# Performance work log

Measured on AMD Instinct MI355X. Metric: run time of the kernel, lower is better.

Reference implementation:

```python
import jax, jax.numpy as jnp
import numpy as np
import math

BS, S, D, H = 16, 512, 1024, 16
DK = D // H
HALF = H // 2
R, GAMMA, EPS = 1.0, 0.1, 1e-6


def _alibi(n_heads, maxpos):
    # n_heads=16 is a power of 2
    start = 2.0 ** (-2.0 ** (-(math.log2(n_heads) - 3)))
    slopes = np.array([start * start ** i for i in range(n_heads)], dtype=np.float32) * -1.0
    pos = np.arange(maxpos)
    rel = np.abs(pos[None, :] - pos[:, None]).astype(np.float32)
    return jnp.asarray((slopes[:, None, None] * rel)[None])  # (1,H,maxpos,maxpos)


def setup_inputs() -> dict:
    key = jax.random.key(0)
    ks = jax.random.split(key, 6)
    sc = 1.0 / math.sqrt(D)
    x = jax.random.normal(ks[0], (BS, S, D), dtype=jnp.float32)
    Wq = jax.random.normal(ks[1], (D, D), dtype=jnp.float32) * sc
    Wk = jax.random.normal(ks[2], (D, D), dtype=jnp.float32) * sc
    Wv = jax.random.normal(ks[3], (D, D), dtype=jnp.float32) * sc
    Wo = jax.random.normal(ks[4], (D, D), dtype=jnp.float32) * sc
    bq = jnp.zeros((D,), jnp.float32)
    bk = jnp.zeros((D,), jnp.float32)
    bv = jnp.zeros((D,), jnp.float32)
    bo = jnp.zeros((D,), jnp.float32)
    alibi = _alibi(H, S)  # pre-sliced to seq_len (original slices [:,:,:S,:S])
    # src_mask for mask=0: np.triu(ones,k=0)==0 -> strictly lower triangular
    mask = jnp.tril(jnp.ones((S, S), dtype=bool), k=-1)[None, None]
    return {"x": x, "Wq": Wq, "bq": bq, "Wk": Wk, "bk": bk, "Wv": Wv,
            "bv": bv, "Wo": Wo, "bo": bo, "alibi": alibi, "mask": mask}


def _map_psi(x, r):
    x_y = jax.nn.sigmoid(x[..., -1])           # (b,h,s)
    return x[..., :-1] * x_y[..., None] * r, x_y * r


def _penumbral(q, k, r=R, gamma=GAMMA, eps=EPS):
    q_x, q_y = _map_psi(q, r)
    k_x, k_y = _map_psi(k, r)
    q_y = q_y[..., :, None]                    # (b,h,s,1)
    k_y = k_y[..., None, :]                    # (b,h,1,s)
    x_q_y = jnp.sqrt(r ** 2 - q_y ** 2 + eps)
    x_k_y = jnp.sqrt(r ** 2 - k_y ** 2 + eps)
    # euclidean cdist over last dim (d_k-1)
    qn = jnp.sum(q_x ** 2, axis=-1)[..., :, None]
    kn = jnp.sum(k_x ** 2, axis=-1)[..., None, :]
    d2 = qn + kn - 2.0 * jnp.einsum('bhqd,bhkd->bhqk', q_x, k_x)
    pd = jnp.sqrt(jnp.maximum(d2, 0.0) + 1e-12)
    lca = jnp.maximum(jnp.maximum(q_y ** 2, k_y ** 2),
                      r ** 2 - ((x_q_y + x_k_y - pd) / 2.0) ** 2)
    lca_out = ((pd ** 2 + k_y ** 2 - q_y ** 2) / (2.0 * pd + eps)) ** 2 + q_y ** 2
    exists = (pd <= x_q_y) | ((pd - x_q_y) ** 2 + k_y ** 2 <= r ** 2)
    return -gamma * jnp.where(exists, lca, lca_out)


def _masked_softmax_zeropad(scores, mask):
    scores = jnp.where(mask, scores, -1e32)
    p = jax.nn.softmax(scores, axis=-1)
    return p.at[:, :, 0, :].set(0.0)  # zero_pad=True (mask==0 branch)


def reference(x, Wq, bq, Wk, bk, Wv, bv, Wo, bo, alibi, mask):
    bs, s, d = x.shape
    q = (x @ Wq.T + bq).reshape(bs, s, H, DK).transpose(0, 2, 1, 3)
    k = (x @ Wk.T + bk).reshape(bs, s, H, DK).transpose(0, 2, 1, 3)
    v = (x @ Wv.T + bv).reshape(bs, s, H, DK).transpose(0, 2, 1, 3)
    inv = 1.0 / math.sqrt(DK)
    # first half heads: standard dot-product attention + alibi
    sc1 = jnp.einsum('bhqd,bhkd->bhqk', q[:, :HALF], k[:, :HALF]) * inv
    sc1 = sc1 + alibi[:, :HALF, :s, :s]
    p1 = _masked_softmax_zeropad(sc1, mask)
    o1 = jnp.einsum('bhqk,bhkd->bhqd', p1, v[:, :HALF])
    # second half heads: penumbral hyperbolic score + alibi
    sc2 = _penumbral(q[:, HALF:], k[:, HALF:]) * inv
    sc2 = sc2 + alibi[:, HALF:, :s, :s]
    p2 = _masked_softmax_zeropad(sc2, mask)
    o2 = jnp.einsum('bhqk,bhkd->bhqd', p2, v[:, HALF:])
    out = jnp.concatenate([o1, o2], axis=1)  # (b,H,s,dk)
    out = out.transpose(0, 2, 1, 3).reshape(bs, s, d)
    return out @ Wo.T + bo
```

## Files before the change

kernel.cpp:

```cpp
#include <hip/hip_runtime.h>
#include <math.h>

#define BS 16
#define S 512
#define D 1024
#define H 16
#define DK 64
#define HALF 8

typedef __attribute__((ext_vector_type(8))) short short8v;
typedef __attribute__((ext_vector_type(4))) float f32x4;
typedef unsigned short ushort_t;

#define L2E 1.4426950408889634f
#define SC_STD (0.125f * L2E)
#define SC_PEN (-0.0125f * L2E)

__device__ __forceinline__ ushort_t f2bf(float f) {
  union { float f; unsigned u; } v; v.f = f;
  unsigned r = v.u + 0x7fffu + ((v.u >> 16) & 1u);
  return (ushort_t)(r >> 16);
}
__device__ __forceinline__ unsigned packbf(float a, float b) {
  return (unsigned)f2bf(a) | ((unsigned)f2bf(b) << 16);
}
__device__ __forceinline__ float bf2f(ushort_t u) {
  union { unsigned u; float f; } v; v.u = ((unsigned)u) << 16;
  return v.f;
}
__device__ __forceinline__ unsigned cvtpk(float lo, float hi) {
  unsigned r;
  asm("v_cvt_pk_bf16_f32 %0, %1, %2" : "=v"(r) : "v"(lo), "v"(hi));
  return r;
}

__device__ __forceinline__ void gload16(const void* g, void* l) {
  __builtin_amdgcn_global_load_lds(
      (const __attribute__((address_space(1))) unsigned int*)g,
      (__attribute__((address_space(3))) unsigned int*)l, 16, 0, 0);
}

#define WAIT_VM(n) asm volatile("s_waitcnt vmcnt(" #n ")" ::: "memory")

__global__ __launch_bounds__(256) void cvt_fused(
    const float* __restrict__ x, const float* __restrict__ Wq,
    const float* __restrict__ Wk, const float* __restrict__ Wv,
    const float* __restrict__ Wo, ushort_t* __restrict__ dst) {
  const int bid = blockIdx.x;
  const float* src;
  int si;
  if (bid < 4096) {
    src = x; si = bid * 256 + threadIdx.x;
  } else {
    const int k = bid - 4096;
    const int w = k >> 9;
    src = (w == 0) ? Wq : (w == 1) ? Wk : (w == 2) ? Wv : Wo;
    si = (k & 511) * 256 + threadIdx.x;
  }
  const int di = bid * 256 + threadIdx.x;
  const float4 a = *(const float4*)(src + (size_t)si * 8);
  const float4 b = *(const float4*)(src + (size_t)si * 8 + 4);
  union { short8v v; unsigned u[4]; } t;
  t.u[0] = packbf(a.x, a.y);
  t.u[1] = packbf(a.z, a.w);
  t.u[2] = packbf(b.x, b.y);
  t.u[3] = packbf(b.z, b.w);
  *(short8v*)(dst + (size_t)di * 8) = t.v;
}

__global__ __launch_bounds__(512) void gemm_qkv(
    const ushort_t* __restrict__ A, const ushort_t* __restrict__ Wcat,
    const float* __restrict__ bq, const float* __restrict__ bk,
    const float* __restrict__ bv, ushort_t* __restrict__ QK,
    ushort_t* __restrict__ Vt, float4* __restrict__ QPn,
    float4* __restrict__ KPn) {
  const int id = blockIdx.x;
  const int xcd = id & 7, r0 = id >> 3;
  const int bn = xcd * 3 + (r0 % 3);
  const int bm = r0 / 3;
  const int tid = threadIdx.x;
  const int lane = tid & 63, wid = tid >> 6;
  const int wr = wid >> 1, wc = wid & 1;
  const int lq = lane & 15, g = lane >> 4;
  const int mat = bn >> 3;

  __shared__ __align__(16) ushort_t sA[2][128 * 64];
  __shared__ __align__(16) ushort_t sB[2][128 * 64];

  f32x4 acc[2][4];
#pragma unroll
  for (int i = 0; i < 2; i++)
#pragma unroll
    for (int j = 0; j < 4; j++) acc[i][j] = (f32x4){0.f, 0.f, 0.f, 0.f};

  auto stage = [&](int buf, int k0) {
#pragma unroll
    for (int ld = 0; ld < 2; ++ld) {
      const int gi = ld * 512 + tid;
      const int row = gi >> 3, slot = gi & 7;
      const int sslot = slot ^ (row & 7);
      gload16(A + (size_t)(bm * 128 + row) * 1024 + k0 + sslot * 8,
              &sA[buf][(size_t)gi * 8]);
      gload16(Wcat + (size_t)(bn * 128 + row) * 1024 + k0 + sslot * 8,
              &sB[buf][(size_t)gi * 8]);
    }
  };

  stage(0, 0);
  WAIT_VM(0);
  __builtin_amdgcn_s_barrier();
  for (int t = 0; t < 16; ++t) {
    if (t < 15) {
      stage((t + 1) & 1, (t + 1) * 64);
      WAIT_VM(4);
    } else {
      WAIT_VM(0);
    }
    __builtin_amdgcn_s_barrier();
    __builtin_amdgcn_sched_barrier(0);
    const int buf = t & 1;
#pragma unroll
    for (int ks = 0; ks < 2; ++ks) {
      short8v af[2], bf[4];
#pragma unroll
      for (int i = 0; i < 2; ++i) {
        const int arow = wr * 32 + i * 16 + lq;
        af[i] = *(const short8v*)&sA[buf][arow * 64 + (((ks * 4 + g) ^ (arow & 7)) * 8)];
      }
#pragma unroll
      for (int j = 0; j < 4; ++j) {
        const int brow = wc * 64 + j * 16 + lq;
        bf[j] = *(const short8v*)&sB[buf][brow * 64 + (((ks * 4 + g) ^ (brow & 7)) * 8)];
      }
#pragma unroll
      for (int i = 0; i < 2; ++i)
#pragma unroll
        for (int j = 0; j < 4; ++j)
          acc[i][j] =
              __builtin_amdgcn_mfma_f32_16x16x32_bf16(af[i], bf[j], acc[i][j], 0, 0, 0);
    }
    __builtin_amdgcn_s_barrier();
  }

  const float* bias = (mat == 0) ? bq : (mat == 1) ? bk : bv;
  const size_t NQKV = (size_t)BS * H * S * DK;

  if (mat < 2) {
    const int headq = (bn & 7) * 2 + wc;
    const bool penq = (headq >= HALF);
    float4* Pn = (mat == 0) ? QPn : KPn;
    ushort_t* Cbase = QK + (size_t)mat * NQKV;
#pragma unroll
    for (int i = 0; i < 2; ++i) {
      const int mb = bm * 128 + wr * 32 + i * 16 + g * 4;
      float cc[4][4];
#pragma unroll
      for (int j = 0; j < 4; ++j) {
        const int n = ((bn & 7) * 128) + wc * 64 + j * 16 + lq;
        const float bvv = bias[n];
#pragma unroll
        for (int r = 0; r < 4; ++r) cc[j][r] = acc[i][j][r] + bvv;
      }
      float yv[4] = {0.f, 0.f, 0.f, 0.f};
      if (penq) {
#pragma unroll
        for (int r = 0; r < 4; ++r) {
          const float last = __shfl(cc[3][r], (lane & 48) + 15, 64);
          yv[r] = 1.0f / (1.0f + __expf(-last));
        }
#pragma unroll
        for (int j = 0; j < 4; ++j)
#pragma unroll
          for (int r = 0; r < 4; ++r) cc[j][r] *= yv[r];
        if (lq == 15) {
#pragma unroll
          for (int r = 0; r < 4; ++r) cc[3][r] = yv[r];
        }
      }
      unsigned pk[4][2];
#pragma unroll
      for (int j = 0; j < 4; ++j) {
        pk[j][0] = cvtpk(cc[j][0], cc[j][1]);
        pk[j][1] = cvtpk(cc[j][2], cc[j][3]);
      }
#pragma unroll
      for (int j = 0; j < 4; ++j) {
        const int n = ((bn & 7) * 128) + wc * 64 + j * 16 + lq;
        ushort_t* base = Cbase +
                         ((((size_t)(mb >> 9) * H + (n >> 6)) * S + (mb & 511)) * DK) +
                         (n & 63);
        base[0] = (ushort_t)pk[j][0];
        base[DK] = (ushort_t)(pk[j][0] >> 16);
        base[2 * DK] = (ushort_t)pk[j][1];
        base[3 * DK] = (ushort_t)(pk[j][1] >> 16);
      }
      if (penq) {
        float sq[4] = {0.f, 0.f, 0.f, 0.f};
#pragma unroll
        for (int j = 0; j < 4; ++j)
#pragma unroll
          for (int r = 0; r < 4; ++r) {
            const unsigned h16 =
                (r & 1) ? (pk[j][r >> 1] >> 16) : (pk[j][r >> 1] & 0xffffu);
            float xr = bf2f((ushort_t)h16);
            if (j == 3 && lq == 15) xr = 0.f;
            sq[r] += xr * xr;
          }
#pragma unroll
        for (int mk = 1; mk <= 8; mk <<= 1)
#pragma unroll
          for (int r = 0; r < 4; ++r) sq[r] += __shfl_xor(sq[r], mk, 64);
        if (lq == 0) {
          const int hh = headq - HALF;
#pragma unroll
          for (int r = 0; r < 4; ++r) {
            const int m = mb + r;
            const int bb = m >> 9, ss = m & 511;
            Pn[((size_t)bb * HALF + hh) * S + ss] = make_float4(
                sq[r], yv[r] * yv[r], sqrtf(1.0f - yv[r] * yv[r] + 1e-6f), 0.f);
          }
        }
      }
    }
  } else {
#pragma unroll
    for (int j = 0; j < 4; ++j) {
      const int n = ((bn & 7) * 128) + wc * 64 + j * 16 + lq;
      const float bvv = bias[n];
#pragma unroll
      for (int i = 0; i < 2; ++i) {
        const int mb = bm * 128 + wr * 32 + i * 16 + g * 4;
        const int bb = mb >> 9, s0 = mb & 511;
        uint2 u;
        u.x = cvtpk(acc[i][j][0] + bvv, acc[i][j][1] + bvv);
        u.y = cvtpk(acc[i][j][2] + bvv, acc[i][j][3] + bvv);
        *(uint2*)(Vt + (((size_t)bb * H + (n >> 6)) * DK + (n & 63)) * S + s0) = u;
      }
    }
  }
}

__global__ __launch_bounds__(512) void gemm_out(
    const ushort_t* __restrict__ A, const ushort_t* __restrict__ B,
    const float* __restrict__ bias, float* __restrict__ C) {
  const int id = blockIdx.x;
  const int bn = id & 7, bm = id >> 3;
  const int tid = threadIdx.x;
  const int lane = tid & 63, wid = tid >> 6;
  const int wr = wid >> 1, wc = wid & 1;
  const int lq = lane & 15, g = lane >> 4;

  __shared__ __align__(16) ushort_t sA[2][128 * 64];
  __shared__ __align__(16) ushort_t sB[2][128 * 64];

  f32x4 acc[2][4];
#pragma unroll
  for (int i = 0; i < 2; i++)
#pragma unroll
    for (int j = 0; j < 4; j++) acc[i][j] = (f32x4){0.f, 0.f, 0.f, 0.f};

  auto stage = [&](int buf, int k0) {
#pragma unroll
    for (int ld = 0; ld < 2; ++ld) {
      const int gi = ld * 512 + tid;
      const int row = gi >> 3, slot = gi & 7;
      const int sslot = slot ^ (row & 7);
      gload16(A + (size_t)(bm * 128 + row) * 1024 + k0 + sslot * 8,
              &sA[buf][(size_t)gi * 8]);
      gload16(B + (size_t)(bn * 128 + row) * 1024 + k0 + sslot * 8,
              &sB[buf][(size_t)gi * 8]);
    }
  };

  stage(0, 0);
  WAIT_VM(0);
  __builtin_amdgcn_s_barrier();
  for (int t = 0; t < 16; ++t) {
    if (t < 15) {
      stage((t + 1) & 1, (t + 1) * 64);
      WAIT_VM(4);
    } else {
      WAIT_VM(0);
    }
    __builtin_amdgcn_s_barrier();
    __builtin_amdgcn_sched_barrier(0);
    const int buf = t & 1;
#pragma unroll
    for (int ks = 0; ks < 2; ++ks) {
      short8v af[2], bf[4];
#pragma unroll
      for (int i = 0; i < 2; ++i) {
        const int arow = wr * 32 + i * 16 + lq;
        af[i] = *(const short8v*)&sA[buf][arow * 64 + (((ks * 4 + g) ^ (arow & 7)) * 8)];
      }
#pragma unroll
      for (int j = 0; j < 4; ++j) {
        const int brow = wc * 64 + j * 16 + lq;
        bf[j] = *(const short8v*)&sB[buf][brow * 64 + (((ks * 4 + g) ^ (brow & 7)) * 8)];
      }
#pragma unroll
      for (int i = 0; i < 2; ++i)
#pragma unroll
        for (int j = 0; j < 4; ++j)
          acc[i][j] =
              __builtin_amdgcn_mfma_f32_16x16x32_bf16(af[i], bf[j], acc[i][j], 0, 0, 0);
    }
    __builtin_amdgcn_s_barrier();
  }

#pragma unroll
  for (int j = 0; j < 4; ++j) {
    const int n = bn * 128 + wc * 64 + j * 16 + lq;
    const float bvv = bias[n];
#pragma unroll
    for (int i = 0; i < 2; ++i) {
      const int mb = bm * 128 + wr * 32 + i * 16 + g * 4;
#pragma unroll
      for (int r = 0; r < 4; ++r)
        C[(size_t)(mb + r) * 1024 + n] = acc[i][j][r] + bvv;
    }
  }
}

template <bool MASK>
__device__ __forceinline__ void attn_tile(
    const char* sKb, const char* sVb, const float4* sPn, const short8v* qf,
    float qn, float qy2, float xqy, bool pen, float slopeL, int qg, int kt0,
    int lq, int g, f32x4* o, float& m, float& lacc) {
  float p[4][4];
  float tmax = -1e30f;
#pragma unroll
  for (int t4 = 0; t4 < 4; ++t4) {
    f32x4 acc = (f32x4){0.f, 0.f, 0.f, 0.f};
    const int row = t4 * 16 + lq;
#pragma unroll
    for (int c = 0; c < 2; ++c) {
      const short8v ka =
          *(const short8v*)(sKb + row * 128 + (((c * 4 + g) ^ (row & 7)) * 16));
      acc = __builtin_amdgcn_mfma_f32_16x16x32_bf16(ka, qf[c], acc, 0, 0, 0);
    }
#pragma unroll
    for (int r = 0; r < 4; ++r) {
      const int kg = kt0 + t4 * 16 + g * 4 + r;
      const float abL = slopeL * (float)(qg - kg);
      float s;
      if (!pen) {
        s = acc[r] * SC_STD + abL;
      } else {
        const float4 kp = sPn[t4 * 16 + g * 4 + r];
        const float kn = kp.x, ky2 = kp.y, xky = kp.z;
        const float d2 = qn + kn - 2.0f * acc[r];
        const float tt = fmaxf(d2, 0.0f) + 1e-12f;
        const float rs = rsqrtf(tt);
        const float pd = tt * rs;
        const float tmp = (xqy + xky - pd) * 0.5f;
        const float lca = fmaxf(fmaxf(qy2, ky2), 1.0f - tmp * tmp);
        const float num = (d2 + ky2 - qy2) * (0.5f * rs);
        const float lout = num * num + qy2;
        const float dxy = pd - xqy;
        const bool ex = (pd <= xqy) || (dxy * dxy + ky2 <= 1.0f);
        s = (ex ? lca : lout) * SC_PEN + abL;
      }
      if (MASK && kg >= qg) s = -1e30f;
      p[t4][r] = s;
      tmax = fmaxf(tmax, s);
    }
  }
  tmax = fmaxf(tmax, __shfl_xor(tmax, 16, 64));
  tmax = fmaxf(tmax, __shfl_xor(tmax, 32, 64));
  const float mnew = fmaxf(m, tmax);
  if (__any(mnew > m)) {
    const float fsc = exp2f(m - mnew);
#pragma unroll
    for (int dt = 0; dt < 4; ++dt) o[dt] *= fsc;
    lacc *= fsc;
    m = mnew;
  }
  float ls = 0.f;
#pragma unroll
  for (int t4 = 0; t4 < 4; ++t4)
#pragma unroll
    for (int r = 0; r < 4; ++r) {
      float pv = exp2f(p[t4][r] - m);
      if (MASK && p[t4][r] < -1e29f) pv = 0.f;
      p[t4][r] = pv;
      ls += pv;
    }
  ls += __shfl_xor(ls, 16, 64);
  ls += __shfl_xor(ls, 32, 64);
  lacc += ls;

  unsigned pk0[4], pk1[4];
#pragma unroll
  for (int t4 = 0; t4 < 4; ++t4) {
    pk0[t4] = cvtpk(p[t4][0], p[t4][1]);
    pk1[t4] = cvtpk(p[t4][2], p[t4][3]);
  }
  const int s0 = lq | (((g * 2) & 3) << 4);
  const int s1 = lq | (((g * 2 + 1) & 3) << 4);
  const bool hi = (g >= 2);
#pragma unroll
  for (int c = 0; c < 2; ++c) {
    const unsigned a0 = (unsigned)__shfl((int)pk0[2 * c], s0, 64);
    const unsigned b0 = (unsigned)__shfl((int)pk0[2 * c + 1], s0, 64);
    const unsigned a1 = (unsigned)__shfl((int)pk1[2 * c], s0, 64);
    const unsigned b1 = (unsigned)__shfl((int)pk1[2 * c + 1], s0, 64);
    const unsigned a2 = (unsigned)__shfl((int)pk0[2 * c], s1, 64);
    const unsigned b2 = (unsigned)__shfl((int)pk0[2 * c + 1], s1, 64);
    const unsigned a3 = (unsigned)__shfl((int)pk1[2 * c], s1, 64);
    const unsigned b3 = (unsigned)__shfl((int)pk1[2 * c + 1], s1, 64);
    union { short8v v; unsigned u[4]; } pb;
    pb.u[0] = hi ? b0 : a0;
    pb.u[1] = hi ? b1 : a1;
    pb.u[2] = hi ? b2 : a2;
    pb.u[3] = hi ? b3 : a3;
#pragma unroll
    for (int dt = 0; dt < 4; ++dt) {
      const int vr = dt * 16 + lq;
      const short8v va =
          *(const short8v*)(sVb + vr * 128 + (((c * 4 + g) ^ (vr & 7)) * 16));
      o[dt] = __builtin_amdgcn_mfma_f32_16x16x32_bf16(va, pb.v, o[dt], 0, 0, 0);
    }
  }
}

__global__ __launch_bounds__(256, 4) void attn_mfma(
    const ushort_t* __restrict__ Qf, const ushort_t* __restrict__ Kf,
    const ushort_t* __restrict__ Vt, const float4* __restrict__ QPn,
    const float4* __restrict__ KPn, ushort_t* __restrict__ O) {
  const int dsp = blockIdx.x;
  const int xcd = dsp & 7, idx = dsp >> 3;
  const int bh = xcd * 32 + (idx & 31);
  const int qb = 7 - (idx >> 5);
  const int b = bh >> 4, h = bh & 15;
  const int tid = threadIdx.x, lane = tid & 63, wid = tid >> 6;
  const int lq = lane & 15, g = lane >> 4;
  const bool pen = (h >= HALF);
  const float slopeL = -exp2f(-0.5f * (float)(h + 1)) * L2E;
  const size_t hoff = ((size_t)b * H + h) * S * DK;
  const ushort_t* Vslab = Vt + hoff;
  const size_t bhh = (size_t)b * HALF + (h & (HALF - 1));

  __shared__ __align__(16) char sK[2][8192];
  __shared__ __align__(16) char sV[2][8192];
  __shared__ __align__(16) float4 sPen[2][64];

  const int qg = qb * 64 + wid * 16 + lq;

  short8v qf[2];
  {
    const ushort_t* qr = Qf + hoff + (size_t)qg * DK;
    qf[0] = *(const short8v*)(qr + g * 8);
    qf[1] = *(const short8v*)(qr + 32 + g * 8);
    if (pen && g == 3) qf[1][7] = 0;
  }
  float qn = 0, qy2 = 0, xqy = 0;
  if (pen) {
    const float4 a = QPn[bhh * S + qg];
    qn = a.x; qy2 = a.y; xqy = a.z;
  }

  const int r8 = lane >> 3;
  const int sl = ((lane & 7) ^ r8) * 8;

  const bool extra = pen && (wid == 0);
  auto stage = [&](int buf, int kt) {
#pragma unroll
    for (int i = 0; i < 2; ++i) {
      const int row = wid * 16 + i * 8 + r8;
      gload16(Kf + hoff + (size_t)(kt * 64 + row) * DK + sl,
              &sK[buf][(wid * 2 + i) * 1024]);
      gload16(Vslab + (size_t)row * S + kt * 64 + sl,
              &sV[buf][(wid * 2 + i) * 1024]);
    }
    if (extra)
      gload16(&KPn[bhh * S + kt * 64 + lane], &sPen[buf][0]);
  };

  f32x4 o[4];
#pragma unroll
  for (int dt = 0; dt < 4; ++dt) o[dt] = (f32x4){0.f, 0.f, 0.f, 0.f};
  float m = -1e30f, l = 0.f;

  stage(0, qb);
  WAIT_VM(0);
  __builtin_amdgcn_s_barrier();
  int cur = 0;
  for (int kt = qb; kt >= 0; --kt) {
    if (kt > 0) {
      stage(cur ^ 1, kt - 1);
      if (extra) { WAIT_VM(5); } else { WAIT_VM(4); }
    } else {
      WAIT_VM(0);
    }
    __builtin_amdgcn_s_barrier();
    __builtin_amdgcn_sched_barrier(0);
    if (kt == qb)
      attn_tile<true>(sK[cur], sV[cur], sPen[cur], qf, qn, qy2, xqy, pen,
                      slopeL, qg, kt * 64, lq, g, o, m, l);
    else
      attn_tile<false>(sK[cur], sV[cur], sPen[cur], qf, qn, qy2, xqy, pen,
                       slopeL, qg, kt * 64, lq, g, o, m, l);
    __builtin_amdgcn_s_barrier();
    cur ^= 1;
  }

  const float invl = (qg == 0) ? 0.f : 1.0f / l;
  ushort_t* orow = O + ((size_t)b * S + qg) * D + h * DK;
#pragma unroll
  for (int dt = 0; dt < 4; ++dt) {
    uint2 u;
    u.x = cvtpk(o[dt][0] * invl, o[dt][1] * invl);
    u.y = cvtpk(o[dt][2] * invl, o[dt][3] * invl);
    *(uint2*)(orow + dt * 16 + g * 4) = u;
  }
}

extern "C" void kernel_launch(void* const* d_in, const int* in_sizes, int n_in,
                              void* d_out, int out_size, void* d_ws,
                              size_t ws_size, hipStream_t stream) {
  (void)in_sizes; (void)n_in; (void)out_size; (void)ws_size;
  const float* x  = (const float*)d_in[0];
  const float* Wq = (const float*)d_in[1];
  const float* bq = (const float*)d_in[2];
  const float* Wk = (const float*)d_in[3];
  const float* bk = (const float*)d_in[4];
  const float* Wv = (const float*)d_in[5];
  const float* bv = (const float*)d_in[6];
  const float* Wo = (const float*)d_in[7];
  const float* bo = (const float*)d_in[8];
  float* out = (float*)d_out;

  const size_t NQKV = (size_t)BS * H * S * DK;
  const size_t NW = (size_t)D * D;
  ushort_t* ws  = (ushort_t*)d_ws;
  ushort_t* Qb  = ws;
  ushort_t* Kbb = Qb + NQKV;
  ushort_t* Vtb = Kbb + NQKV;
  ushort_t* Ob  = Vtb + NQKV;
  ushort_t* xb  = Ob + NQKV;
  ushort_t* Wqb = xb + NQKV;
  ushort_t* Wkb = Wqb + NW;
  ushort_t* Wvb = Wkb + NW;
  ushort_t* Wob = Wvb + NW;
  float4* QPn = (float4*)(Wob + NW);
  float4* KPn = QPn + (size_t)BS * HALF * S;

  cvt_fused<<<dim3(4096 + 4 * 512), 256, 0, stream>>>(x, Wq, Wk, Wv, Wo, xb);
  gemm_qkv<<<dim3(1536), 512, 0, stream>>>(xb, Wqb, bq, bk, bv, Qb, Vtb, QPn,
                                           KPn);
  attn_mfma<<<dim3(2048), 256, 0, stream>>>(Qb, Kbb, Vtb, QPn, KPn, Ob);
  gemm_out<<<dim3(512), 512, 0, stream>>>(Ob, Wob, bo, out);
}
```

Before: 147.3 us.

## Restructure QKV GEMM to 256x128 tiles with triple-buffered ping-pong schedule

The QKV projection GEMM now uses 256-row M tiles, so each wave computes a 64x64 output block, and the grid is halved to 768 blocks. Global-to-LDS staging is triple buffered with a prefetch distance of two, and the LDS reads are split into quarter-tile fragments interleaved with MFMA groups. Barriers and s_setprio bracket each MFMA group to overlap LDS traffic with matrix math across waves. In exchange it uses more LDS (about 144KB) and accumulator registers, which lowers occupancy, and fewer blocks may underfill the CUs.

```diff
diff --git a/kernel.cpp b/kernel.cpp
--- a/kernel.cpp
+++ b/kernel.cpp
@@ -41,6 +41,8 @@
 }
 
 #define WAIT_VM(n) asm volatile("s_waitcnt vmcnt(" #n ")" ::: "memory")
+#define SBAR() __builtin_amdgcn_s_barrier()
+#define SCHED() __builtin_amdgcn_sched_barrier(0)
 
 __global__ __launch_bounds__(256) void cvt_fused(
     const float* __restrict__ x, const float* __restrict__ Wq,
@@ -78,85 +80,115 @@
   const int xcd = id & 7, r0 = id >> 3;
   const int bn = xcd * 3 + (r0 % 3);
   const int bm = r0 / 3;
+  const int mat = bn >> 3;
   const int tid = threadIdx.x;
   const int lane = tid & 63, wid = tid >> 6;
-  const int wr = wid >> 1, wc = wid & 1;
+  const int wm = wid >> 1, wn = wid & 1;
   const int lq = lane & 15, g = lane >> 4;
-  const int mat = bn >> 3;
-
-  __shared__ __align__(16) ushort_t sA[2][128 * 64];
-  __shared__ __align__(16) ushort_t sB[2][128 * 64];
-
-  f32x4 acc[2][4];
-#pragma unroll
-  for (int i = 0; i < 2; i++)
+
+  __shared__ __align__(16) ushort_t sA[3][256 * 64];
+  __shared__ __align__(16) ushort_t sB[3][128 * 64];
+
+  f32x4 acc[4][4];
+#pragma unroll
+  for (int i = 0; i < 4; i++)
 #pragma unroll
     for (int j = 0; j < 4; j++) acc[i][j] = (f32x4){0.f, 0.f, 0.f, 0.f};
 
-  auto stage = [&](int buf, int k0) {
-#pragma unroll
-    for (int ld = 0; ld < 2; ++ld) {
-      const int gi = ld * 512 + tid;
-      const int row = gi >> 3, slot = gi & 7;
-      const int sslot = slot ^ (row & 7);
-      gload16(A + (size_t)(bm * 128 + row) * 1024 + k0 + sslot * 8,
-              &sA[buf][(size_t)gi * 8]);
-      gload16(Wcat + (size_t)(bn * 128 + row) * 1024 + k0 + sslot * 8,
-              &sB[buf][(size_t)gi * 8]);
-    }
+  const ushort_t* aSrc[4];
+  const ushort_t* bSrc[2];
+#pragma unroll
+  for (int ld = 0; ld < 4; ++ld) {
+    const int gi = ld * 512 + tid;
+    const int row = gi >> 3, slot = gi & 7;
+    aSrc[ld] = A + (size_t)(bm * 256 + row) * 1024 + ((slot ^ (row & 7)) * 8);
+  }
+#pragma unroll
+  for (int ld = 0; ld < 2; ++ld) {
+    const int gi = ld * 512 + tid;
+    const int row = gi >> 3, slot = gi & 7;
+    bSrc[ld] =
+        Wcat + (size_t)(bn * 128 + row) * 1024 + ((slot ^ (row & 7)) * 8);
+  }
+
+  auto stage = [&](int k, int kt) {
+#pragma unroll
+    for (int ld = 0; ld < 4; ++ld)
+      gload16(aSrc[ld] + kt * 64, &sA[k][(size_t)(ld * 512 + tid) * 8]);
+#pragma unroll
+    for (int ld = 0; ld < 2; ++ld)
+      gload16(bSrc[ld] + kt * 64, &sB[k][(size_t)(ld * 512 + tid) * 8]);
   };
 
+#define DSA(AF, IH, BI)                                                      \
+  _Pragma("unroll") for (int i = 0; i < 2; ++i)                              \
+  _Pragma("unroll") for (int ks = 0; ks < 2; ++ks) {                         \
+    const int row_ = wm * 64 + ((IH)*2 + i) * 16 + lq;                       \
+    AF[i][ks] = *(const short8v*)&sA[BI]                                     \
+        [row_ * 64 + (((ks * 4 + g) ^ (row_ & 7)) * 8)];                     \
+  }
+#define DSB(BF, JH, BI)                                                      \
+  _Pragma("unroll") for (int j = 0; j < 2; ++j)                              \
+  _Pragma("unroll") for (int ks = 0; ks < 2; ++ks) {                         \
+    const int row_ = wn * 64 + ((JH)*2 + j) * 16 + lq;                       \
+    BF[j][ks] = *(const short8v*)&sB[BI]                                     \
+        [row_ * 64 + (((ks * 4 + g) ^ (row_ & 7)) * 8)];                     \
+  }
+#define MM(IH, JH, AF, BF)                                                   \
+  _Pragma("unroll") for (int ks = 0; ks < 2; ++ks)                           \
+  _Pragma("unroll") for (int i = 0; i < 2; ++i)                              \
+  _Pragma("unroll") for (int j = 0; j < 2; ++j)                              \
+    acc[(IH)*2 + i][(JH)*2 + j] = __builtin_amdgcn_mfma_f32_16x16x32_bf16(   \
+        AF[i][ks], BF[j][ks], acc[(IH)*2 + i][(JH)*2 + j], 0, 0, 0);
+
   stage(0, 0);
-  WAIT_VM(0);
-  __builtin_amdgcn_s_barrier();
+  stage(1, 1);
+
   for (int t = 0; t < 16; ++t) {
-    if (t < 15) {
-      stage((t + 1) & 1, (t + 1) * 64);
-      WAIT_VM(4);
-    } else {
-      WAIT_VM(0);
-    }
-    __builtin_amdgcn_s_barrier();
-    __builtin_amdgcn_sched_barrier(0);
-    const int buf = t & 1;
-#pragma unroll
-    for (int ks = 0; ks < 2; ++ks) {
-      short8v af[2], bf[4];
-#pragma unroll
-      for (int i = 0; i < 2; ++i) {
-        const int arow = wr * 32 + i * 16 + lq;
-        af[i] = *(const short8v*)&sA[buf][arow * 64 + (((ks * 4 + g) ^ (arow & 7)) * 8)];
-      }
-#pragma unroll
-      for (int j = 0; j < 4; ++j) {
-        const int brow = wc * 64 + j * 16 + lq;
-        bf[j] = *(const short8v*)&sB[buf][brow * 64 + (((ks * 4 + g) ^ (brow & 7)) * 8)];
-      }
-#pragma unroll
-      for (int i = 0; i < 2; ++i)
-#pragma unroll
-        for (int j = 0; j < 4; ++j)
-          acc[i][j] =
-              __builtin_amdgcn_mfma_f32_16x16x32_bf16(af[i], bf[j], acc[i][j], 0, 0, 0);
-    }
-    __builtin_amdgcn_s_barrier();
+    const int bi = t % 3;
+    if (t == 15) { WAIT_VM(0); } else { WAIT_VM(6); }
+    SBAR();
+    SCHED();
+    if (t + 2 < 16) stage((t + 2) % 3, t + 2);
+    short8v a0[2][2], a1[2][2], b0[2][2], b1[2][2];
+    DSA(a0, 0, bi);
+    DSB(b0, 0, bi);
+    SBAR();
+    __builtin_amdgcn_s_setprio(1);
+    MM(0, 0, a0, b0);
+    __builtin_amdgcn_s_setprio(0);
+    DSB(b1, 1, bi);
+    SBAR();
+    __builtin_amdgcn_s_setprio(1);
+    MM(0, 1, a0, b1);
+    __builtin_amdgcn_s_setprio(0);
+    DSA(a1, 1, bi);
+    SBAR();
+    __builtin_amdgcn_s_setprio(1);
+    MM(1, 1, a1, b1);
+    __builtin_amdgcn_s_setprio(0);
+    DSB(b0, 0, bi);
+    SBAR();
+    __builtin_amdgcn_s_setprio(1);
+    MM(1, 0, a1, b0);
+    __builtin_amdgcn_s_setprio(0);
   }
 
   const float* bias = (mat == 0) ? bq : (mat == 1) ? bk : bv;
   const size_t NQKV = (size_t)BS * H * S * DK;
 
   if (mat < 2) {
-    const int headq = (bn & 7) * 2 + wc;
+    const int headq = (bn & 7) * 2 + wn;
     const bool penq = (headq >= HALF);
     float4* Pn = (mat == 0) ? QPn : KPn;
     ushort_t* Cbase = QK + (size_t)mat * NQKV;
 #pragma unroll
-    for (int i = 0; i < 2; ++i) {
-      const int mb = bm * 128 + wr * 32 + i * 16 + g * 4;
+    for (int i = 0; i < 4; ++i) {
+      const int mb = bm * 256 + wm * 64 + i * 16 + g * 4;
       float cc[4][4];
 #pragma unroll
       for (int j = 0; j < 4; ++j) {
-        const int n = ((bn & 7) * 128) + wc * 64 + j * 16 + lq;
+        const int n = ((bn & 7) * 128) + wn * 64 + j * 16 + lq;
         const float bvv = bias[n];
 #pragma unroll
         for (int r = 0; r < 4; ++r) cc[j][r] = acc[i][j][r] + bvv;
@@ -185,7 +217,7 @@
       }
 #pragma unroll
       for (int j = 0; j < 4; ++j) {
-        const int n = ((bn & 7) * 128) + wc * 64 + j * 16 + lq;
+        const int n = ((bn & 7) * 128) + wn * 64 + j * 16 + lq;
         ushort_t* base = Cbase +
                          ((((size_t)(mb >> 9) * H + (n >> 6)) * S + (mb & 511)) * DK) +
                          (n & 63);
@@ -225,11 +257,11 @@
   } else {
 #pragma unroll
     for (int j = 0; j < 4; ++j) {
-      const int n = ((bn & 7) * 128) + wc * 64 + j * 16 + lq;
+      const int n = ((bn & 7) * 128) + wn * 64 + j * 16 + lq;
       const float bvv = bias[n];
 #pragma unroll
-      for (int i = 0; i < 2; ++i) {
-        const int mb = bm * 128 + wr * 32 + i * 16 + g * 4;
+      for (int i = 0; i < 4; ++i) {
+        const int mb = bm * 256 + wm * 64 + i * 16 + g * 4;
         const int bb = mb >> 9, s0 = mb & 511;
         uint2 u;
         u.x = cvtpk(acc[i][j][0] + bvv, acc[i][j][1] + bvv);
@@ -238,6 +270,9 @@
       }
     }
   }
+#undef DSA
+#undef DSB
+#undef MM
 }
 
 __global__ __launch_bounds__(512) void gemm_out(
@@ -274,7 +309,7 @@
 
   stage(0, 0);
   WAIT_VM(0);
-  __builtin_amdgcn_s_barrier();
+  SBAR();
   for (int t = 0; t < 16; ++t) {
     if (t < 15) {
       stage((t + 1) & 1, (t + 1) * 64);
@@ -282,8 +317,8 @@
     } else {
       WAIT_VM(0);
     }
-    __builtin_amdgcn_s_barrier();
-    __builtin_amdgcn_sched_barrier(0);
+    SBAR();
+    SCHED();
     const int buf = t & 1;
 #pragma unroll
     for (int ks = 0; ks < 2; ++ks) {
@@ -305,7 +340,7 @@
           acc[i][j] =
               __builtin_amdgcn_mfma_f32_16x16x32_bf16(af[i], bf[j], acc[i][j], 0, 0, 0);
     }
-    __builtin_amdgcn_s_barrier();
+    SBAR();
   }
 
 #pragma unroll
@@ -484,7 +519,7 @@
 
   stage(0, qb);
   WAIT_VM(0);
-  __builtin_amdgcn_s_barrier();
+  SBAR();
   int cur = 0;
   for (int kt = qb; kt >= 0; --kt) {
     if (kt > 0) {
@@ -493,15 +528,15 @@
     } else {
       WAIT_VM(0);
     }
-    __builtin_amdgcn_s_barrier();
-    __builtin_amdgcn_sched_barrier(0);
+    SBAR();
+    SCHED();
     if (kt == qb)
       attn_tile<true>(sK[cur], sV[cur], sPen[cur], qf, qn, qy2, xqy, pen,
                       slopeL, qg, kt * 64, lq, g, o, m, l);
     else
       attn_tile<false>(sK[cur], sV[cur], sPen[cur], qf, qn, qy2, xqy, pen,
                        slopeL, qg, kt * 64, lq, g, o, m, l);
-    __builtin_amdgcn_s_barrier();
+    SBAR();
     cur ^= 1;
   }
 
@@ -547,8 +582,8 @@
   float4* KPn = QPn + (size_t)BS * HALF * S;
 
   cvt_fused<<<dim3(4096 + 4 * 512), 256, 0, stream>>>(x, Wq, Wk, Wv, Wo, xb);
-  gemm_qkv<<<dim3(1536), 512, 0, stream>>>(xb, Wqb, bq, bk, bv, Qb, Vtb, QPn,
-                                           KPn);
+  gemm_qkv<<<dim3(768), 512, 0, stream>>>(xb, Wqb, bq, bk, bv, Qb, Vtb, QPn,
+                                          KPn);
   attn_mfma<<<dim3(2048), 256, 0, stream>>>(Qb, Kbb, Vtb, QPn, KPn, Ob);
   gemm_out<<<dim3(512), 512, 0, stream>>>(Ob, Wob, bo, out);
 }
```

Result: slower. 166.2 us (+12.8%).
